# Kernel tuning notes

Measured on AMD Instinct MI355X. Metric: run time of the kernel, lower is better.

Reference implementation:

```python
import jax, jax.numpy as jnp
import numpy as np

B, T, C = 4, 2048, 1024
N_HEAD = 16
HEAD_DIM = C // N_HEAD


def setup_inputs() -> dict:
    key = jax.random.key(0)
    k1, k2, k3 = jax.random.split(key, 3)
    scale = 1.0 / np.sqrt(C)
    return {
        "x": jax.random.normal(k1, (B, T, C), dtype=jnp.float32),
        "W_attn": jax.random.normal(k2, (C, 3 * C), dtype=jnp.float32) * scale,
        "b_attn": jnp.zeros((3 * C,), dtype=jnp.float32),
        "W_proj": jax.random.normal(k3, (C, C), dtype=jnp.float32) * scale,
        "b_proj": jnp.zeros((C,), dtype=jnp.float32),
    }


def reference(x, W_attn, b_attn, W_proj, b_proj):
    Bt, Tt, Ct = x.shape
    qkv = x @ W_attn + b_attn                      # [B,T,3C]
    q, k, v = jnp.split(qkv, 3, axis=-1)
    # [B,T,C] -> [B,H,T,D]
    def heads(t):
        return t.reshape(Bt, Tt, N_HEAD, HEAD_DIM).transpose(0, 2, 1, 3)
    q, k, v = heads(q), heads(k), heads(v)
    att = jnp.einsum("bhqd,bhkd->bhqk", q, k) * (1.0 / np.sqrt(HEAD_DIM))
    causal = jnp.tril(jnp.ones((Tt, Tt), dtype=bool))
    att = jnp.where(causal, att, jnp.finfo(att.dtype).min)
    att = jax.nn.softmax(att, axis=-1)
    # dropout = 0.0 (eval mode): identity
    y = jnp.einsum("bhqk,bhkd->bhqd", att, v)      # [B,H,T,D]
    y = y.transpose(0, 2, 1, 3).reshape(Bt, Tt, Ct)
    return y @ W_proj + b_proj
```

## Files before the change

kernel.cpp:

```cpp
#include <hip/hip_runtime.h>
#include <hip/hip_bf16.h>
#include <cstdint>

#define B_SZ 4
#define T_SZ 2048
#define C_SZ 1024
#define H_SZ 16
#define D_SZ 64
#define BT_SZ (B_SZ * T_SZ)
#define C3_SZ (3 * C_SZ)
#define NKC (C_SZ / 32)

typedef __attribute__((ext_vector_type(8))) short bf16x8;
typedef __attribute__((ext_vector_type(4))) float f32x4;
typedef __attribute__((ext_vector_type(4))) unsigned short ushort4v;
typedef __attribute__((ext_vector_type(4))) unsigned int uint4v;

typedef __attribute__((address_space(3))) unsigned int lds_u32;
typedef __attribute__((address_space(1))) const unsigned int glb_u32;

__device__ __forceinline__ unsigned short f2bf(float f) {
  unsigned u = __builtin_bit_cast(unsigned, f);
  u += 0x7fffu + ((u >> 16) & 1u);
  return (unsigned short)(u >> 16);
}

__device__ __forceinline__ unsigned packbf2(float lo, float hi) {
  return __builtin_amdgcn_perm(__builtin_bit_cast(unsigned, hi),
                               __builtin_bit_cast(unsigned, lo), 0x07060302u);
}

__device__ __forceinline__ void gll16(const unsigned short* g,
                                      unsigned short* l) {
  __builtin_amdgcn_global_load_lds((glb_u32*)g, (lds_u32*)l, 16, 0, 0);
}


__device__ __forceinline__ void pack_x_task(const float* __restrict__ x,
                                            unsigned short* __restrict__ Af,
                                            int task, int lane) {
  const int quad = lane >> 4, n = lane & 15;
  const int tb = task >> 5, kc = task & 31;
  const float* src = x + (size_t)(tb * 16 + n) * C_SZ + kc * 32 + quad * 8;
  float4 a = *(const float4*)src;
  float4 b = *(const float4*)(src + 4);
  ushort4v o0, o1;
  o0[0] = f2bf(a.x); o0[1] = f2bf(a.y); o0[2] = f2bf(a.z); o0[3] = f2bf(a.w);
  o1[0] = f2bf(b.x); o1[1] = f2bf(b.y); o1[2] = f2bf(b.z); o1[3] = f2bf(b.w);
  unsigned short* dst = Af + ((size_t)((tb * NKC + kc) * 4 + quad) * 16 + n) * 8;
  *(ushort4v*)dst = o0;
  *(ushort4v*)(dst + 4) = o1;
}

__device__ __forceinline__ void pack_w_task(const float* __restrict__ W,
                                            unsigned short* __restrict__ Wb,
                                            int N, int task, int lane) {
  const int quad = lane >> 4, n = lane & 15;
  const int nt = task >> 5, kc = task & 31;
  const int col = nt * 16 + n;
  const int k0 = kc * 32 + quad * 8;
  ushort4v o0, o1;
#pragma unroll
  for (int i = 0; i < 4; ++i) o0[i] = f2bf(W[(size_t)(k0 + i) * N + col]);
#pragma unroll
  for (int i = 0; i < 4; ++i) o1[i] = f2bf(W[(size_t)(k0 + 4 + i) * N + col]);
  unsigned short* dst = Wb + ((size_t)((nt * NKC + kc) * 4 + quad) * 16 + n) * 8;
  *(ushort4v*)dst = o0;
  *(ushort4v*)(dst + 4) = o1;
}

__global__ __launch_bounds__(256) void pack_all(
    const float* __restrict__ x, const float* __restrict__ Wa,
    const float* __restrict__ Wp, unsigned short* __restrict__ Af,
    unsigned short* __restrict__ Wab, unsigned short* __restrict__ Wpb) {
  const int bx = blockIdx.x;
  const int sub = threadIdx.x >> 6;
  const int lane = threadIdx.x & 63;
  if (bx < 4096) {
    pack_x_task(x, Af, bx * 4 + sub, lane);
  } else if (bx < 4096 + 1536) {
    pack_w_task(Wa, Wab, C3_SZ, (bx - 4096) * 4 + sub, lane);
  } else {
    pack_w_task(Wp, Wpb, C_SZ, (bx - 5632) * 4 + sub, lane);
  }
}

__device__ __forceinline__ void gemm128_mainloop(
    const unsigned short* __restrict__ A, const unsigned short* __restrict__ B,
    int tbB, int ntB, unsigned short* smem, f32x4 acc[4][4]) {
  const int tid = threadIdx.x;
  const int w = tid >> 6, lane = tid & 63;
  const int quad = lane >> 4, n = lane & 15;
  const int wr = w >> 1, wc = w & 1;
  unsigned short* smemA = smem;
  unsigned short* smemB = smem + 8192;

  for (int kc0 = 0; kc0 < NKC; kc0 += 2) {
#pragma unroll
    for (int i2 = 0; i2 < 2; ++i2) {
      const int i = 2 * w + i2;
      const unsigned short* gA =
          A + ((size_t)(tbB + i) * NKC + kc0) * 512 + lane * 8;
      const unsigned short* gB =
          B + ((size_t)(ntB + i) * NKC + kc0) * 512 + lane * 8;
      gll16(gA, smemA + i * 1024);
      gll16(gA + 512, smemA + i * 1024 + 512);
      gll16(gB, smemB + i * 1024);
      gll16(gB + 512, smemB + i * 1024 + 512);
    }
    __syncthreads();
#pragma unroll
    for (int kcl = 0; kcl < 2; ++kcl) {
      bf16x8 af[4], bfr[4];
#pragma unroll
      for (int m = 0; m < 4; ++m)
        af[m] = *(const bf16x8*)(smemA + (wr * 4 + m) * 1024 +
                                 (kcl * 4 + quad) * 128 + n * 8);
#pragma unroll
      for (int nn = 0; nn < 4; ++nn)
        bfr[nn] = *(const bf16x8*)(smemB + (wc * 4 + nn) * 1024 +
                                   (kcl * 4 + quad) * 128 + n * 8);
#pragma unroll
      for (int m = 0; m < 4; ++m)
#pragma unroll
        for (int nn = 0; nn < 4; ++nn)
          acc[m][nn] = __builtin_amdgcn_mfma_f32_16x16x32_bf16(
              af[m], bfr[nn], acc[m][nn], 0, 0, 0);
    }
    __syncthreads();
  }
}

__global__ __launch_bounds__(256) void qkv_mfma(
    const unsigned short* __restrict__ Af, const unsigned short* __restrict__ Wab,
    const float* __restrict__ bias, unsigned short* __restrict__ Qf,
    unsigned short* __restrict__ Kf, unsigned short* __restrict__ Vf) {
  __shared__ unsigned short smem[16384];
  const int tid = threadIdx.x;
  const int w = tid >> 6, lane = tid & 63;
  const int quad = lane >> 4, n = lane & 15;
  const int wr = w >> 1, wc = w & 1;
  const int f = blockIdx.x;
  const int xcd = f & 7, i = f >> 3;
  const int by = xcd * 8 + (i / 24);
  const int bx = i % 24;
  f32x4 acc[4][4];
#pragma unroll
  for (int m = 0; m < 4; ++m)
#pragma unroll
    for (int nn = 0; nn < 4; ++nn) acc[m][nn] = (f32x4){0.f, 0.f, 0.f, 0.f};

  gemm128_mainloop(Af, Wab, by * 8, bx * 8, smem, acc);

  const int cb = bx * 128 + wc * 64;
  const int which = cb >> 10;
  const int h = (cb & 1023) >> 6;
  const int gr0 = by * 128 + wr * 64;
  const int b = gr0 >> 11;
  const int t0 = gr0 & 2047;
  const size_t bhoff = (size_t)(b * H_SZ + h) * (T_SZ * D_SZ);
  float bfl[4];
#pragma unroll
  for (int nn = 0; nn < 4; ++nn) bfl[nn] = bias[cb + nn * 16 + n];

  if (which < 2) {
    unsigned short* dst = ((which == 0) ? Qf : Kf) + bhoff;
    const float scl = (which == 0) ? 0.18033688f : 1.0f;
#pragma unroll
    for (int m = 0; m < 4; ++m) {
      const int tb = (t0 + m * 16) >> 4;
#pragma unroll
      for (int nn = 0; nn < 4; ++nn) {
        const int dc = nn >> 1;
        const int qd = (nn & 1) * 2 + (n >> 3);
        const int jq = n & 7;
#pragma unroll
        for (int r = 0; r < 4; ++r) {
          const int nq = quad * 4 + r;
          dst[((size_t)((tb * 2 + dc) * 4 + qd)) * 128 + nq * 8 + jq] =
              f2bf((acc[m][nn][r] + bfl[nn]) * scl);
        }
      }
    }
  } else {
    unsigned short* dst = Vf + bhoff;
    const int gb0 = t0 >> 5;
#pragma unroll
    for (int m = 0; m < 4; ++m) {
      const int gb = gb0 + (m >> 1);
#pragma unroll
      for (int nn = 0; nn < 4; ++nn) {
#pragma unroll
        for (int r = 0; r < 4; ++r) {
          dst[((size_t)((gb * 4 + nn) * 4 + quad)) * 128 + n * 8 + (m & 1) * 4 + r] =
              f2bf(acc[m][nn][r] + bfl[nn]);
        }
      }
    }
  }
}

__global__ __launch_bounds__(256) void proj_mfma(
    const unsigned short* __restrict__ Yf, const unsigned short* __restrict__ Wpb,
    const float* __restrict__ bias, float* __restrict__ out) {
  __shared__ unsigned short smem[16384];
  const int tid = threadIdx.x;
  const int w = tid >> 6, lane = tid & 63;
  const int quad = lane >> 4, n = lane & 15;
  const int wr = w >> 1, wc = w & 1;
  const int f = blockIdx.x;
  const int xcd = f & 7, i = f >> 3;
  const int by = xcd * 8 + (i / 8);
  const int bx = i % 8;
  f32x4 acc[4][4];
#pragma unroll
  for (int m = 0; m < 4; ++m)
#pragma unroll
    for (int nn = 0; nn < 4; ++nn) acc[m][nn] = (f32x4){0.f, 0.f, 0.f, 0.f};

  gemm128_mainloop(Yf, Wpb, by * 8, bx * 8, smem, acc);

  const int cb = bx * 128 + wc * 64;
  const int gr0 = by * 128 + wr * 64;
  float bfl[4];
#pragma unroll
  for (int nn = 0; nn < 4; ++nn) bfl[nn] = bias[cb + nn * 16 + n];
#pragma unroll
  for (int m = 0; m < 4; ++m)
#pragma unroll
    for (int nn = 0; nn < 4; ++nn)
#pragma unroll
      for (int r = 0; r < 4; ++r)
        out[(size_t)(gr0 + m * 16 + quad * 4 + r) * C_SZ + cb + nn * 16 + n] =
            acc[m][nn][r] + bfl[nn];
}

__global__ __launch_bounds__(64) void attn_mfma(
    const unsigned short* __restrict__ Qf,
    const unsigned short* __restrict__ Kf,
    const unsigned short* __restrict__ Vf, unsigned short* __restrict__ Yf) {
  const int lane = threadIdx.x;
  const int quad = lane >> 4;
  const int n = lane & 15;
  const int bx = blockIdx.x;
  const int qt = 31 - (bx >> 6);
  const int bh = bx & 63;
  const int b = bh >> 4, h = bh & 15;
  const int wq0 = qt * 64;
  const size_t bhoff = (size_t)bh * (T_SZ * D_SZ);
  const bf16x8* Qp = (const bf16x8*)(Qf + bhoff);
  const bf16x8* Kp = (const bf16x8*)(Kf + bhoff);
  const bf16x8* Vp = (const bf16x8*)(Vf + bhoff);

  bf16x8 qfr[4][2];
#pragma unroll
  for (int m = 0; m < 4; ++m) {
    const int tb = (wq0 >> 4) + m;
#pragma unroll
    for (int dc = 0; dc < 2; ++dc)
      qfr[m][dc] = Qp[((tb * 2 + dc) * 4 + quad) * 16 + n];
  }

  bf16x8 kfr[4][2], vfr[2][4];
  f32x4 O[4][4];
  f32x4 ls[4];
#pragma unroll
  for (int m = 0; m < 4; ++m) {
    ls[m] = (f32x4){0.f, 0.f, 0.f, 0.f};
#pragma unroll
    for (int dv = 0; dv < 4; ++dv) O[m][dv] = (f32x4){0.f, 0.f, 0.f, 0.f};
  }

#pragma unroll
  for (int s = 0; s < 4; ++s) {
    kfr[s][0] = Kp[((s * 2 + 0) * 4 + quad) * 16 + n];
    kfr[s][1] = Kp[((s * 2 + 1) * 4 + quad) * 16 + n];
  }
#pragma unroll
  for (int g = 0; g < 2; ++g)
#pragma unroll
    for (int dv = 0; dv < 4; ++dv)
      vfr[g][dv] = Vp[((g * 4 + dv) * 4 + quad) * 16 + n];

  for (int kt = 0; kt < qt; ++kt) {
#pragma unroll
    for (int m = 0; m < 4; ++m) {
      f32x4 st[4];
#pragma unroll
      for (int s = 0; s < 4; ++s) {
        f32x4 z = {0.f, 0.f, 0.f, 0.f};
        z = __builtin_amdgcn_mfma_f32_16x16x32_bf16(kfr[s][0], qfr[m][0], z, 0, 0, 0);
        z = __builtin_amdgcn_mfma_f32_16x16x32_bf16(kfr[s][1], qfr[m][1], z, 0, 0, 0);
        st[s] = z;
      }
      if (m == 3) {
        const int tb0 = (kt + 1) * 4;
#pragma unroll
        for (int s = 0; s < 4; ++s) {
          kfr[s][0] = Kp[(((tb0 + s) * 2 + 0) * 4 + quad) * 16 + n];
          kfr[s][1] = Kp[(((tb0 + s) * 2 + 1) * 4 + quad) * 16 + n];
        }
      }
      uint4v pw[2];
#pragma unroll
      for (int s = 0; s < 4; ++s) {
        float pr[4];
#pragma unroll
        for (int r = 0; r < 4; ++r) {
          pr[r] = __builtin_amdgcn_exp2f(st[s][r]);
          ls[m][r] += pr[r];
        }
        pw[s >> 1][(s & 1) * 2 + 0] = packbf2(pr[0], pr[1]);
        pw[s >> 1][(s & 1) * 2 + 1] = packbf2(pr[2], pr[3]);
      }
#pragma unroll
      for (int g = 0; g < 2; ++g) {
        const bf16x8 pg = __builtin_bit_cast(bf16x8, pw[g]);
#pragma unroll
        for (int dv = 0; dv < 4; ++dv)
          O[m][dv] = __builtin_amdgcn_mfma_f32_16x16x32_bf16(
              pg, vfr[g][dv], O[m][dv], 0, 0, 0);
      }
      if (m == 3) {
        const int gb0 = (kt + 1) * 2;
#pragma unroll
        for (int g = 0; g < 2; ++g)
#pragma unroll
          for (int dv = 0; dv < 4; ++dv)
            vfr[g][dv] = Vp[(((gb0 + g) * 4 + dv) * 4 + quad) * 16 + n];
      }
    }
  }

  {
#pragma unroll
    for (int m = 0; m < 4; ++m) {
      f32x4 st[4];
#pragma unroll
      for (int s = 0; s < 4; ++s) {
        f32x4 z = {0.f, 0.f, 0.f, 0.f};
        if (s <= m) {
          z = __builtin_amdgcn_mfma_f32_16x16x32_bf16(kfr[s][0], qfr[m][0], z, 0, 0, 0);
          z = __builtin_amdgcn_mfma_f32_16x16x32_bf16(kfr[s][1], qfr[m][1], z, 0, 0, 0);
        }
        st[s] = z;
      }
      uint4v pw[2] = {(uint4v){0, 0, 0, 0}, (uint4v){0, 0, 0, 0}};
#pragma unroll
      for (int s = 0; s < 4; ++s) {
        if (s <= m) {
          float pr[4];
#pragma unroll
          for (int r = 0; r < 4; ++r) {
            float v = st[s][r];
            if (s == m && quad * 4 + r > n) v = -1e30f;
            pr[r] = __builtin_amdgcn_exp2f(v);
            ls[m][r] += pr[r];
          }
          pw[s >> 1][(s & 1) * 2 + 0] = packbf2(pr[0], pr[1]);
          pw[s >> 1][(s & 1) * 2 + 1] = packbf2(pr[2], pr[3]);
        }
      }
#pragma unroll
      for (int g = 0; g < 2; ++g) {
        if (g * 2 <= m) {
          const bf16x8 pg = __builtin_bit_cast(bf16x8, pw[g]);
#pragma unroll
          for (int dv = 0; dv < 4; ++dv)
            O[m][dv] = __builtin_amdgcn_mfma_f32_16x16x32_bf16(
                pg, vfr[g][dv], O[m][dv], 0, 0, 0);
        }
      }
    }
  }

#pragma unroll
  for (int m = 0; m < 4; ++m) {
    float lt = ls[m][0] + ls[m][1] + ls[m][2] + ls[m][3];
    lt += __shfl_xor(lt, 16);
    lt += __shfl_xor(lt, 32);
    const float inv = 1.0f / lt;
    float iv[4];
#pragma unroll
    for (int r = 0; r < 4; ++r) iv[r] = __shfl(inv, quad * 4 + r);
    const int tb = (b * T_SZ + wq0 + m * 16) >> 4;
#pragma unroll
    for (int dv = 0; dv < 4; ++dv) {
      const int kc = h * 2 + (dv >> 1);
      const int qa = (dv & 1) * 2 + (n >> 3);
      const int ja = n & 7;
#pragma unroll
      for (int r = 0; r < 4; ++r) {
        const int na = quad * 4 + r;
        Yf[((size_t)((tb * NKC + kc) * 4 + qa)) * 128 + na * 8 + ja] =
            f2bf(O[m][dv][r] * iv[r]);
      }
    }
  }
}

extern "C" void kernel_launch(void* const* d_in, const int* in_sizes, int n_in,
                              void* d_out, int out_size, void* d_ws,
                              size_t ws_size, hipStream_t stream) {
  const float* x = (const float*)d_in[0];
  const float* W_attn = (const float*)d_in[1];
  const float* b_attn = (const float*)d_in[2];
  const float* W_proj = (const float*)d_in[3];
  const float* b_proj = (const float*)d_in[4];
  float* out = (float*)d_out;

  const size_t perbf = (size_t)B_SZ * H_SZ * T_SZ * D_SZ;
  unsigned short* Af = (unsigned short*)d_ws;
  unsigned short* Wab = Af + (size_t)BT_SZ * C_SZ;
  unsigned short* Wpb = Wab + (size_t)C_SZ * C3_SZ;
  unsigned short* Qf = Wpb + (size_t)C_SZ * C_SZ;
  unsigned short* Kf = Qf + perbf;
  unsigned short* Vf = Kf + perbf;
  unsigned short* Yf = Vf + perbf;

  pack_all<<<6144, 256, 0, stream>>>(x, W_attn, W_proj, Af, Wab, Wpb);
  qkv_mfma<<<1536, 256, 0, stream>>>(Af, Wab, b_attn, Qf, Kf, Vf);
  attn_mfma<<<dim3(32 * B_SZ * H_SZ), 64, 0, stream>>>(Qf, Kf, Vf, Yf);
  proj_mfma<<<512, 256, 0, stream>>>(Yf, Wpb, b_proj, out);
}
```

Baseline: 223.6 us.

## Use 256x128 tiles with 8-wave double-buffered ping-pong GEMM mainloop

Replaces the synchronous 128x128 GEMM mainloop with a 128x256 tile run by 8 waves. It uses double-buffered LDS and 64-wide K tiles, and interleaves global-to-LDS prefetch with MFMA quadrants behind many barriers and raised priority. This aims to hide global load latency and raise per-block data reuse in the QKV and projection GEMMs. The cost is larger LDS use (96KB), fewer blocks, and a fragile hand-tuned vmcnt schedule.

```diff
diff --git a/kernel.cpp b/kernel.cpp
--- a/kernel.cpp
+++ b/kernel.cpp
@@ -10,6 +10,7 @@
 #define BT_SZ (B_SZ * T_SZ)
 #define C3_SZ (3 * C_SZ)
 #define NKC (C_SZ / 32)
+#define NKT (C_SZ / 64)
 
 typedef __attribute__((ext_vector_type(8))) short bf16x8;
 typedef __attribute__((ext_vector_type(4))) float f32x4;
@@ -85,74 +86,119 @@
   }
 }
 
-__device__ __forceinline__ void gemm128_mainloop(
+__device__ __forceinline__ void gemm_8ph_mainloop(
     const unsigned short* __restrict__ A, const unsigned short* __restrict__ B,
     int tbB, int ntB, unsigned short* smem, f32x4 acc[4][4]) {
   const int tid = threadIdx.x;
   const int w = tid >> 6, lane = tid & 63;
   const int quad = lane >> 4, n = lane & 15;
-  const int wr = w >> 1, wc = w & 1;
-  unsigned short* smemA = smem;
-  unsigned short* smemB = smem + 8192;
-
-  for (int kc0 = 0; kc0 < NKC; kc0 += 2) {
-#pragma unroll
-    for (int i2 = 0; i2 < 2; ++i2) {
-      const int i = 2 * w + i2;
-      const unsigned short* gA =
-          A + ((size_t)(tbB + i) * NKC + kc0) * 512 + lane * 8;
-      const unsigned short* gB =
-          B + ((size_t)(ntB + i) * NKC + kc0) * 512 + lane * 8;
-      gll16(gA, smemA + i * 1024);
-      gll16(gA + 512, smemA + i * 1024 + 512);
-      gll16(gB, smemB + i * 1024);
-      gll16(gB + 512, smemB + i * 1024 + 512);
-    }
-    __syncthreads();
-#pragma unroll
-    for (int kcl = 0; kcl < 2; ++kcl) {
-      bf16x8 af[4], bfr[4];
-#pragma unroll
-      for (int m = 0; m < 4; ++m)
-        af[m] = *(const bf16x8*)(smemA + (wr * 4 + m) * 1024 +
-                                 (kcl * 4 + quad) * 128 + n * 8);
-#pragma unroll
-      for (int nn = 0; nn < 4; ++nn)
-        bfr[nn] = *(const bf16x8*)(smemB + (wc * 4 + nn) * 1024 +
-                                   (kcl * 4 + quad) * 128 + n * 8);
-#pragma unroll
-      for (int m = 0; m < 4; ++m)
-#pragma unroll
-        for (int nn = 0; nn < 4; ++nn)
-          acc[m][nn] = __builtin_amdgcn_mfma_f32_16x16x32_bf16(
-              af[m], bfr[nn], acc[m][nn], 0, 0, 0);
-    }
-    __syncthreads();
-  }
-}
-
-__global__ __launch_bounds__(256) void qkv_mfma(
+  const int wr = w >> 2, wc = w & 3;
+
+  auto stageA = [&](int buf, int t, int h) {
+    gll16(A + ((size_t)(tbB + h * 4 + (w >> 1)) * NKC + t * 2 + (w & 1)) * 512 +
+              lane * 8,
+          smem + buf * 24576 + ((h * 4 + (w >> 1)) * 2 + (w & 1)) * 512);
+  };
+  auto stageB = [&](int buf, int t, int h) {
+    const unsigned short* src =
+        B + ((size_t)(ntB + h * 8 + w) * NKC + t * 2) * 512 + lane * 8;
+    unsigned short* dst = smem + buf * 24576 + 8192 + (h * 8 + w) * 1024;
+    gll16(src, dst);
+    gll16(src + 512, dst + 512);
+  };
+
+  auto ldA = [&](int buf, int mh, bf16x8 af[2][2]) {
+#pragma unroll
+    for (int mi = 0; mi < 2; ++mi)
+#pragma unroll
+      for (int kc = 0; kc < 2; ++kc)
+        af[mi][kc] = *(const bf16x8*)(smem + buf * 24576 +
+            ((wr * 4 + mh * 2 + mi) * 2 + kc) * 512 + quad * 128 + n * 8);
+  };
+  auto ldB = [&](int buf, bf16x8 bfr[4][2]) {
+#pragma unroll
+    for (int nn = 0; nn < 4; ++nn)
+#pragma unroll
+      for (int kc = 0; kc < 2; ++kc)
+        bfr[nn][kc] = *(const bf16x8*)(smem + buf * 24576 + 8192 +
+            ((wc * 4 + nn) * 2 + kc) * 512 + quad * 128 + n * 8);
+  };
+  auto mmaQ = [&](int mh, int nh, bf16x8 af[2][2], bf16x8 bfr[4][2]) {
+    __builtin_amdgcn_s_setprio(1);
+#pragma unroll
+    for (int mi = 0; mi < 2; ++mi)
+#pragma unroll
+      for (int nj = 0; nj < 2; ++nj)
+#pragma unroll
+        for (int kc = 0; kc < 2; ++kc)
+          acc[mh * 2 + mi][nh * 2 + nj] =
+              __builtin_amdgcn_mfma_f32_16x16x32_bf16(
+                  af[mi][kc], bfr[nh * 2 + nj][kc],
+                  acc[mh * 2 + mi][nh * 2 + nj], 0, 0, 0);
+    __builtin_amdgcn_s_setprio(0);
+  };
+
+  stageB(0, 0, 0); stageB(0, 0, 1); stageA(0, 0, 0); stageA(0, 0, 1);
+  stageB(1, 1, 0); stageB(1, 1, 1); stageA(1, 1, 0);
+  asm volatile("s_waitcnt vmcnt(5)" ::: "memory");
+  __builtin_amdgcn_s_barrier();
+
+  auto tileStep = [&](int t, int cur, bool s1, bool s2) {
+    const int nxt = cur ^ 1;
+    bf16x8 af[2][2], bfr[4][2];
+    ldA(cur, 0, af);
+    ldB(cur, bfr);
+    if (s1) stageA(nxt, t + 1, 1);
+    __builtin_amdgcn_s_barrier();
+    mmaQ(0, 0, af, bfr);
+    __builtin_amdgcn_s_barrier();
+    if (s2) stageB(cur, t + 2, 0);
+    __builtin_amdgcn_s_barrier();
+    mmaQ(0, 1, af, bfr);
+    __builtin_amdgcn_s_barrier();
+    ldA(cur, 1, af);
+    if (s2) stageB(cur, t + 2, 1);
+    __builtin_amdgcn_s_barrier();
+    mmaQ(1, 1, af, bfr);
+    __builtin_amdgcn_s_barrier();
+    if (s2) stageA(cur, t + 2, 0);
+    __builtin_amdgcn_s_barrier();
+    mmaQ(1, 0, af, bfr);
+    if (s2) {
+      asm volatile("s_waitcnt vmcnt(5)" ::: "memory");
+    } else if (s1) {
+      asm volatile("s_waitcnt vmcnt(0)" ::: "memory");
+    }
+    __builtin_amdgcn_s_barrier();
+  };
+
+  for (int t = 0; t < NKT - 2; ++t) tileStep(t, t & 1, true, true);
+  tileStep(NKT - 2, (NKT - 2) & 1, true, false);
+  tileStep(NKT - 1, (NKT - 1) & 1, false, false);
+}
+
+__global__ __launch_bounds__(512) void qkv_mfma(
     const unsigned short* __restrict__ Af, const unsigned short* __restrict__ Wab,
     const float* __restrict__ bias, unsigned short* __restrict__ Qf,
     unsigned short* __restrict__ Kf, unsigned short* __restrict__ Vf) {
-  __shared__ unsigned short smem[16384];
+  __shared__ __align__(16) unsigned short smem[49152];
   const int tid = threadIdx.x;
   const int w = tid >> 6, lane = tid & 63;
   const int quad = lane >> 4, n = lane & 15;
-  const int wr = w >> 1, wc = w & 1;
+  const int wr = w >> 2, wc = w & 3;
   const int f = blockIdx.x;
   const int xcd = f & 7, i = f >> 3;
-  const int by = xcd * 8 + (i / 24);
-  const int bx = i % 24;
+  const int by = xcd * 8 + (i / 12);
+  const int bx = i % 12;
   f32x4 acc[4][4];
 #pragma unroll
   for (int m = 0; m < 4; ++m)
 #pragma unroll
     for (int nn = 0; nn < 4; ++nn) acc[m][nn] = (f32x4){0.f, 0.f, 0.f, 0.f};
 
-  gemm128_mainloop(Af, Wab, by * 8, bx * 8, smem, acc);
-
-  const int cb = bx * 128 + wc * 64;
+  gemm_8ph_mainloop(Af, Wab, by * 8, bx * 16, smem, acc);
+
+  const int cb = bx * 256 + wc * 64;
   const int which = cb >> 10;
   const int h = (cb & 1023) >> 6;
   const int gr0 = by * 128 + wr * 64;
@@ -200,27 +246,27 @@
   }
 }
 
-__global__ __launch_bounds__(256) void proj_mfma(
+__global__ __launch_bounds__(512) void proj_mfma(
     const unsigned short* __restrict__ Yf, const unsigned short* __restrict__ Wpb,
     const float* __restrict__ bias, float* __restrict__ out) {
-  __shared__ unsigned short smem[16384];
+  __shared__ __align__(16) unsigned short smem[49152];
   const int tid = threadIdx.x;
   const int w = tid >> 6, lane = tid & 63;
   const int quad = lane >> 4, n = lane & 15;
-  const int wr = w >> 1, wc = w & 1;
+  const int wr = w >> 2, wc = w & 3;
   const int f = blockIdx.x;
   const int xcd = f & 7, i = f >> 3;
-  const int by = xcd * 8 + (i / 8);
-  const int bx = i % 8;
+  const int by = xcd * 8 + (i / 4);
+  const int bx = i % 4;
   f32x4 acc[4][4];
 #pragma unroll
   for (int m = 0; m < 4; ++m)
 #pragma unroll
     for (int nn = 0; nn < 4; ++nn) acc[m][nn] = (f32x4){0.f, 0.f, 0.f, 0.f};
 
-  gemm128_mainloop(Yf, Wpb, by * 8, bx * 8, smem, acc);
-
-  const int cb = bx * 128 + wc * 64;
+  gemm_8ph_mainloop(Yf, Wpb, by * 8, bx * 16, smem, acc);
+
+  const int cb = bx * 256 + wc * 64;
   const int gr0 = by * 128 + wr * 64;
   float bfl[4];
 #pragma unroll
@@ -419,7 +465,7 @@
   unsigned short* Yf = Vf + perbf;
 
   pack_all<<<6144, 256, 0, stream>>>(x, W_attn, W_proj, Af, Wab, Wpb);
-  qkv_mfma<<<1536, 256, 0, stream>>>(Af, Wab, b_attn, Qf, Kf, Vf);
+  qkv_mfma<<<768, 512, 0, stream>>>(Af, Wab, b_attn, Qf, Kf, Vf);
   attn_mfma<<<dim3(32 * B_SZ * H_SZ), 64, 0, stream>>>(Qf, Kf, Vf, Yf);
-  proj_mfma<<<512, 256, 0, stream>>>(Yf, Wpb, b_proj, out);
-}
+  proj_mfma<<<256, 512, 0, stream>>>(Yf, Wpb, b_proj, out);
+}
```

New measurement: 224.7 us. Within noise of the previous version (+0.5%).

## Split attention KV range across two waves per block and merge via LDS

Applied to the files above, without the earlier changes.

The attention kernel now launches two waves per query tile. Each wave handles half of the off-diagonal key tiles, and the second wave also handles the diagonal tile. Partial O and row sums are combined through shared memory before normalization and the write. This is meant to halve the serial KV loop length per block and reduce tail imbalance from causal work, at the cost of LDS traffic, a barrier, and one wave sitting idle during the epilogue. Separately, the V store in the QKV kernel is vectorized to 4-element writes.

```diff
diff --git a/kernel.cpp b/kernel.cpp
--- a/kernel.cpp
+++ b/kernel.cpp
@@ -190,11 +190,11 @@
       const int gb = gb0 + (m >> 1);
 #pragma unroll
       for (int nn = 0; nn < 4; ++nn) {
-#pragma unroll
-        for (int r = 0; r < 4; ++r) {
-          dst[((size_t)((gb * 4 + nn) * 4 + quad)) * 128 + n * 8 + (m & 1) * 4 + r] =
-              f2bf(acc[m][nn][r] + bfl[nn]);
-        }
+        ushort4v o;
+#pragma unroll
+        for (int r = 0; r < 4; ++r) o[r] = f2bf(acc[m][nn][r] + bfl[nn]);
+        *(ushort4v*)(dst + ((size_t)((gb * 4 + nn) * 4 + quad)) * 128 +
+                     n * 8 + (m & 1) * 4) = o;
       }
     }
   }
@@ -235,11 +235,15 @@
             acc[m][nn][r] + bfl[nn];
 }
 
-__global__ __launch_bounds__(64) void attn_mfma(
+__global__ __launch_bounds__(128) void attn_mfma(
     const unsigned short* __restrict__ Qf,
     const unsigned short* __restrict__ Kf,
     const unsigned short* __restrict__ Vf, unsigned short* __restrict__ Yf) {
-  const int lane = threadIdx.x;
+  __shared__ f32x4 sO[64][16];
+  __shared__ f32x4 sLs[64][4];
+  const int tid = threadIdx.x;
+  const int wv = tid >> 6;
+  const int lane = tid & 63;
   const int quad = lane >> 4;
   const int n = lane & 15;
   const int bx = blockIdx.x;
@@ -252,6 +256,11 @@
   const bf16x8* Kp = (const bf16x8*)(Kf + bhoff);
   const bf16x8* Vp = (const bf16x8*)(Vf + bhoff);
 
+  const int nA = (qt + 1) >> 1;
+  const int kbeg = wv ? nA : 0;
+  const int kend = wv ? qt : nA;
+  const bool active = (wv == 1) || (nA > 0);
+
   bf16x8 qfr[4][2];
 #pragma unroll
   for (int m = 0; m < 4; ++m) {
@@ -271,68 +280,70 @@
     for (int dv = 0; dv < 4; ++dv) O[m][dv] = (f32x4){0.f, 0.f, 0.f, 0.f};
   }
 
-#pragma unroll
-  for (int s = 0; s < 4; ++s) {
-    kfr[s][0] = Kp[((s * 2 + 0) * 4 + quad) * 16 + n];
-    kfr[s][1] = Kp[((s * 2 + 1) * 4 + quad) * 16 + n];
-  }
-#pragma unroll
-  for (int g = 0; g < 2; ++g)
-#pragma unroll
-    for (int dv = 0; dv < 4; ++dv)
-      vfr[g][dv] = Vp[((g * 4 + dv) * 4 + quad) * 16 + n];
-
-  for (int kt = 0; kt < qt; ++kt) {
-#pragma unroll
-    for (int m = 0; m < 4; ++m) {
-      f32x4 st[4];
-#pragma unroll
-      for (int s = 0; s < 4; ++s) {
-        f32x4 z = {0.f, 0.f, 0.f, 0.f};
-        z = __builtin_amdgcn_mfma_f32_16x16x32_bf16(kfr[s][0], qfr[m][0], z, 0, 0, 0);
-        z = __builtin_amdgcn_mfma_f32_16x16x32_bf16(kfr[s][1], qfr[m][1], z, 0, 0, 0);
-        st[s] = z;
-      }
-      if (m == 3) {
-        const int tb0 = (kt + 1) * 4;
+  if (active) {
+#pragma unroll
+    for (int s = 0; s < 4; ++s) {
+      kfr[s][0] = Kp[(((kbeg * 4 + s) * 2 + 0) * 4 + quad) * 16 + n];
+      kfr[s][1] = Kp[(((kbeg * 4 + s) * 2 + 1) * 4 + quad) * 16 + n];
+    }
+#pragma unroll
+    for (int g = 0; g < 2; ++g)
+#pragma unroll
+      for (int dv = 0; dv < 4; ++dv)
+        vfr[g][dv] = Vp[(((kbeg * 2 + g) * 4 + dv) * 4 + quad) * 16 + n];
+
+    for (int kt = kbeg; kt < kend; ++kt) {
+#pragma unroll
+      for (int m = 0; m < 4; ++m) {
+        f32x4 st[4];
 #pragma unroll
         for (int s = 0; s < 4; ++s) {
-          kfr[s][0] = Kp[(((tb0 + s) * 2 + 0) * 4 + quad) * 16 + n];
-          kfr[s][1] = Kp[(((tb0 + s) * 2 + 1) * 4 + quad) * 16 + n];
-        }
-      }
-      uint4v pw[2];
-#pragma unroll
-      for (int s = 0; s < 4; ++s) {
-        float pr[4];
-#pragma unroll
-        for (int r = 0; r < 4; ++r) {
-          pr[r] = __builtin_amdgcn_exp2f(st[s][r]);
-          ls[m][r] += pr[r];
-        }
-        pw[s >> 1][(s & 1) * 2 + 0] = packbf2(pr[0], pr[1]);
-        pw[s >> 1][(s & 1) * 2 + 1] = packbf2(pr[2], pr[3]);
-      }
-#pragma unroll
-      for (int g = 0; g < 2; ++g) {
-        const bf16x8 pg = __builtin_bit_cast(bf16x8, pw[g]);
-#pragma unroll
-        for (int dv = 0; dv < 4; ++dv)
-          O[m][dv] = __builtin_amdgcn_mfma_f32_16x16x32_bf16(
-              pg, vfr[g][dv], O[m][dv], 0, 0, 0);
-      }
-      if (m == 3) {
-        const int gb0 = (kt + 1) * 2;
-#pragma unroll
-        for (int g = 0; g < 2; ++g)
+          f32x4 z = {0.f, 0.f, 0.f, 0.f};
+          z = __builtin_amdgcn_mfma_f32_16x16x32_bf16(kfr[s][0], qfr[m][0], z, 0, 0, 0);
+          z = __builtin_amdgcn_mfma_f32_16x16x32_bf16(kfr[s][1], qfr[m][1], z, 0, 0, 0);
+          st[s] = z;
+        }
+        if (m == 3) {
+          const int tb0 = (kt + 1) * 4;
+#pragma unroll
+          for (int s = 0; s < 4; ++s) {
+            kfr[s][0] = Kp[(((tb0 + s) * 2 + 0) * 4 + quad) * 16 + n];
+            kfr[s][1] = Kp[(((tb0 + s) * 2 + 1) * 4 + quad) * 16 + n];
+          }
+        }
+        uint4v pw[2];
+#pragma unroll
+        for (int s = 0; s < 4; ++s) {
+          float pr[4];
+#pragma unroll
+          for (int r = 0; r < 4; ++r) {
+            pr[r] = __builtin_amdgcn_exp2f(st[s][r]);
+            ls[m][r] += pr[r];
+          }
+          pw[s >> 1][(s & 1) * 2 + 0] = packbf2(pr[0], pr[1]);
+          pw[s >> 1][(s & 1) * 2 + 1] = packbf2(pr[2], pr[3]);
+        }
+#pragma unroll
+        for (int g = 0; g < 2; ++g) {
+          const bf16x8 pg = __builtin_bit_cast(bf16x8, pw[g]);
 #pragma unroll
           for (int dv = 0; dv < 4; ++dv)
-            vfr[g][dv] = Vp[(((gb0 + g) * 4 + dv) * 4 + quad) * 16 + n];
-      }
-    }
-  }
-
-  {
+            O[m][dv] = __builtin_amdgcn_mfma_f32_16x16x32_bf16(
+                pg, vfr[g][dv], O[m][dv], 0, 0, 0);
+        }
+        if (m == 3) {
+          const int gb0 = (kt + 1) * 2;
+#pragma unroll
+          for (int g = 0; g < 2; ++g)
+#pragma unroll
+            for (int dv = 0; dv < 4; ++dv)
+              vfr[g][dv] = Vp[(((gb0 + g) * 4 + dv) * 4 + quad) * 16 + n];
+        }
+      }
+    }
+  }
+
+  if (wv == 1) {
 #pragma unroll
     for (int m = 0; m < 4; ++m) {
       f32x4 st[4];
@@ -372,28 +383,43 @@
         }
       }
     }
-  }
-
-#pragma unroll
-  for (int m = 0; m < 4; ++m) {
-    float lt = ls[m][0] + ls[m][1] + ls[m][2] + ls[m][3];
-    lt += __shfl_xor(lt, 16);
-    lt += __shfl_xor(lt, 32);
-    const float inv = 1.0f / lt;
-    float iv[4];
-#pragma unroll
-    for (int r = 0; r < 4; ++r) iv[r] = __shfl(inv, quad * 4 + r);
-    const int tb = (b * T_SZ + wq0 + m * 16) >> 4;
-#pragma unroll
-    for (int dv = 0; dv < 4; ++dv) {
-      const int kc = h * 2 + (dv >> 1);
-      const int qa = (dv & 1) * 2 + (n >> 3);
-      const int ja = n & 7;
-#pragma unroll
-      for (int r = 0; r < 4; ++r) {
-        const int na = quad * 4 + r;
-        Yf[((size_t)((tb * NKC + kc) * 4 + qa)) * 128 + na * 8 + ja] =
-            f2bf(O[m][dv][r] * iv[r]);
+#pragma unroll
+    for (int m = 0; m < 4; ++m) {
+      sLs[lane][m] = ls[m];
+#pragma unroll
+      for (int dv = 0; dv < 4; ++dv) sO[lane][m * 4 + dv] = O[m][dv];
+    }
+  }
+  __syncthreads();
+
+  if (wv == 0) {
+#pragma unroll
+    for (int m = 0; m < 4; ++m) {
+      ls[m] += sLs[lane][m];
+#pragma unroll
+      for (int dv = 0; dv < 4; ++dv) O[m][dv] += sO[lane][m * 4 + dv];
+    }
+#pragma unroll
+    for (int m = 0; m < 4; ++m) {
+      float lt = ls[m][0] + ls[m][1] + ls[m][2] + ls[m][3];
+      lt += __shfl_xor(lt, 16);
+      lt += __shfl_xor(lt, 32);
+      const float inv = 1.0f / lt;
+      float iv[4];
+#pragma unroll
+      for (int r = 0; r < 4; ++r) iv[r] = __shfl(inv, quad * 4 + r);
+      const int tb = (b * T_SZ + wq0 + m * 16) >> 4;
+#pragma unroll
+      for (int dv = 0; dv < 4; ++dv) {
+        const int kc = h * 2 + (dv >> 1);
+        const int qa = (dv & 1) * 2 + (n >> 3);
+        const int ja = n & 7;
+#pragma unroll
+        for (int r = 0; r < 4; ++r) {
+          const int na = quad * 4 + r;
+          Yf[((size_t)((tb * NKC + kc) * 4 + qa)) * 128 + na * 8 + ja] =
+              f2bf(O[m][dv][r] * iv[r]);
+        }
       }
     }
   }
@@ -420,6 +446,6 @@
 
   pack_all<<<6144, 256, 0, stream>>>(x, W_attn, W_proj, Af, Wab, Wpb);
   qkv_mfma<<<1536, 256, 0, stream>>>(Af, Wab, b_attn, Qf, Kf, Vf);
-  attn_mfma<<<dim3(32 * B_SZ * H_SZ), 64, 0, stream>>>(Qf, Kf, Vf, Yf);
+  attn_mfma<<<dim3(32 * B_SZ * H_SZ), 128, 0, stream>>>(Qf, Kf, Vf, Yf);
   proj_mfma<<<512, 256, 0, stream>>>(Yf, Wpb, b_proj, out);
 }
```

Measured after the change: 230.1 us. +2.9%, slower.
